# Performance work log

Hardware: AMD Instinct MI355X
Metric: run time of the kernel (lower is better)

The kernel has to match this reference:

```python
import jax, jax.numpy as jnp
import numpy as np

B, C, H, W = 16, 256, 32, 32
N_HEAD, DIM_HEAD = 8, 32  # dim_hidden = 256 == C


def setup_inputs() -> dict:
    key = jax.random.key(0)
    ks = jax.random.split(key, 9)
    s = 1.0 / np.sqrt(C)
    return {
        "x": jax.random.normal(ks[0], (B, C, H, W), dtype=jnp.float32),
        "w_q": jax.random.normal(ks[1], (C, C), dtype=jnp.float32) * s,
        "b_q": jnp.zeros((C,), dtype=jnp.float32),
        "w_k": jax.random.normal(ks[2], (C, C), dtype=jnp.float32) * s,
        "b_k": jnp.zeros((C,), dtype=jnp.float32),
        "w_v": jax.random.normal(ks[3], (C, C), dtype=jnp.float32) * s,
        "b_v": jnp.zeros((C,), dtype=jnp.float32),
        "w_o": jax.random.normal(ks[4], (C, C), dtype=jnp.float32) * s,
        "b_o": jnp.zeros((C,), dtype=jnp.float32),
    }


def reference(x, w_q, b_q, w_k, b_k, w_v, b_v, w_o, b_o):
    b, c, h, w = x.shape
    L = h * w
    scale = DIM_HEAD ** (-0.5)
    xf = x.reshape(b, c, L)  # [b, c, L]

    def proj(wm, bm):
        # 1x1 conv == per-position linear over channels
        y = jnp.einsum('oc,bcl->bol', wm, xf) + bm[None, :, None]
        return y.reshape(b, N_HEAD, DIM_HEAD, L)

    q = proj(w_q, b_q) * scale
    k = proj(w_k, b_k)
    v = proj(w_v, b_v)

    sim = jnp.einsum('bndl,bndm->bnlm', q, k)           # [b, n, L, L]
    att = jax.nn.softmax(sim, axis=-1)
    out = jnp.einsum('bnlm,bndm->bndl', att, v)         # [b, n, d, L]
    out = out.reshape(b, c, L)
    out = jnp.einsum('oc,bcl->bol', w_o, out) + b_o[None, :, None]
    return out.reshape(b, c, h, w)
```

## Files before the change

kernel.cpp:

```cpp
#include <hip/hip_runtime.h>
#include <hip/hip_bf16.h>
#include <math.h>

namespace {
constexpr int B_ = 16, C_ = 256, L_ = 1024, NH_ = 8, DH_ = 32;

typedef __attribute__((ext_vector_type(8))) short short8v;
typedef __attribute__((ext_vector_type(4))) float float4v;

__device__ __forceinline__ short f2bf(float f) {
    unsigned u = __builtin_bit_cast(unsigned, f);
    u += 0x7fffu + ((u >> 16) & 1u);
    return (short)(u >> 16);
}
__device__ __forceinline__ unsigned pkrn(float a, float b) {
    float2 f; f.x = a; f.y = b;
    __hip_bfloat162 h = __float22bfloat162_rn(f);
    unsigned u;
    __builtin_memcpy(&u, &h, sizeof(u));
    return u;
}
__device__ __forceinline__ void gld16(const short* g, short* l) {
    __builtin_amdgcn_global_load_lds(
        (const __attribute__((address_space(1))) unsigned*)g,
        (__attribute__((address_space(3))) unsigned*)l, 16, 0, 0);
}

__global__ __launch_bounds__(256, 4) void qkv_kernel(
    const float* __restrict__ X,
    const float* __restrict__ wq, const float* __restrict__ wk, const float* __restrict__ wv_,
    const float* __restrict__ bias0, const float* __restrict__ bias1, const float* __restrict__ bias2,
    float qscale, short* __restrict__ out0, short* __restrict__ out1, short* __restrict__ out2)
{
    const int lt = blockIdx.x, ot = blockIdx.y, b = blockIdx.z;
    const int t = threadIdx.x, wv = t >> 6, lane = t & 63;
    const int quad = lane >> 4, c = lane & 15;
    const int wo = (wv & 1) * 64;
    const int wl = (wv >> 1) * 32;

    __shared__ short sA[128 * 64];
    __shared__ short sB[64 * 64];

    float4v acc[4][2];
#pragma unroll
    for (int i = 0; i < 4; ++i)
#pragma unroll
        for (int j = 0; j < 2; ++j) acc[i][j] = (float4v)0.f;

    const int typ = ot >> 1;
    const float* Wsrc = (typ == 0) ? wq : (typ == 1) ? wk : wv_;
    const float* Wbase = Wsrc + (size_t)((ot & 1) * 128) * 256;

    const int srow = t >> 3, sseg = t & 7;
    const int seg = sseg ^ (srow & 7);

    for (int kk = 0; kk < 4; ++kk) {
        __syncthreads();
#pragma unroll
        for (int e = 0; e < 4; ++e) {
            const float* p = Wbase + (size_t)(e * 32 + srow) * 256 + kk * 64 + seg * 8;
            const float4 a0 = *(const float4*)p;
            const float4 a1 = *(const float4*)(p + 4);
            unsigned pk[4];
            pk[0] = pkrn(a0.x, a0.y); pk[1] = pkrn(a0.z, a0.w);
            pk[2] = pkrn(a1.x, a1.y); pk[3] = pkrn(a1.z, a1.w);
            *(uint4*)&sA[(e * 256 + t) * 8] = *(uint4*)pk;
        }
        {
            const int lrow = t & 63, w8 = t >> 6;
            const float* xcol = X + ((size_t)b * C_ + kk * 64 + w8 * 16) * L_ + lt * 64 + lrow;
            float vvv[16];
#pragma unroll
            for (int j = 0; j < 16; ++j) vvv[j] = xcol[(size_t)j * L_];
            unsigned pk[8];
#pragma unroll
            for (int j = 0; j < 8; ++j) pk[j] = pkrn(vvv[2 * j], vvv[2 * j + 1]);
            *(uint4*)&sB[(lrow * 8 + ((2 * w8)     ^ (lrow & 7))) * 8] = *(uint4*)&pk[0];
            *(uint4*)&sB[(lrow * 8 + ((2 * w8 + 1) ^ (lrow & 7))) * 8] = *(uint4*)&pk[4];
        }
        __syncthreads();

#pragma unroll
        for (int kc2 = 0; kc2 < 2; ++kc2) {
            short8v af[4], bf[2];
#pragma unroll
            for (int i = 0; i < 4; ++i) {
                const int row = wo + 16 * i + c;
                af[i] = *(const short8v*)&sA[row * 64 + (((kc2 * 4 + quad) ^ (c & 7)) * 8)];
            }
#pragma unroll
            for (int j = 0; j < 2; ++j) {
                const int row = wl + 16 * j + c;
                bf[j] = *(const short8v*)&sB[row * 64 + (((kc2 * 4 + quad) ^ (c & 7)) * 8)];
            }
#pragma unroll
            for (int i = 0; i < 4; ++i)
#pragma unroll
                for (int j = 0; j < 2; ++j)
                    acc[i][j] = __builtin_amdgcn_mfma_f32_16x16x32_bf16(af[i], bf[j], acc[i][j], 0, 0, 0);
        }
    }

    const int chbase = (ot & 1) * 128 + wo;
    const float* bp = (typ == 0) ? bias0 : (typ == 1) ? bias1 : bias2;
    const float sc = (typ == 0) ? qscale : 1.f;
    short* outp = (typ == 0) ? out0 : (typ == 1) ? out1 : out2;
    if (typ < 2) {
#pragma unroll
        for (int i = 0; i < 4; ++i) {
            const int ch0 = chbase + 16 * i + quad * 4;
            const int head = ch0 >> 5, d0 = ch0 & 31;
            float bias[4];
#pragma unroll
            for (int r = 0; r < 4; ++r) bias[r] = bp[ch0 + r];
#pragma unroll
            for (int j = 0; j < 2; ++j) {
                const int l = lt * 64 + wl + 16 * j + c;
                short4 sv;
                sv.x = f2bf((acc[i][j][0] + bias[0]) * sc);
                sv.y = f2bf((acc[i][j][1] + bias[1]) * sc);
                sv.z = f2bf((acc[i][j][2] + bias[2]) * sc);
                sv.w = f2bf((acc[i][j][3] + bias[3]) * sc);
                *(short4*)&outp[(((size_t)b * NH_ + head) * L_ + l) * 32 + d0] = sv;
            }
        }
    } else {
#pragma unroll
        for (int i = 0; i < 4; ++i)
#pragma unroll
            for (int r = 0; r < 4; ++r) {
                const int ch = chbase + 16 * i + quad * 4 + r;
                const float bias = bp[ch];
#pragma unroll
                for (int j = 0; j < 2; ++j)
                    outp[((size_t)b * C_ + ch) * L_ + lt * 64 + wl + 16 * j + c] =
                        f2bf(acc[i][j][r] + bias);
            }
    }
}

__global__ __launch_bounds__(256, 4) void ogemm_kernel(
    const float* __restrict__ Wo,
    const short* __restrict__ Bsrc,
    const float* __restrict__ bias,
    float* __restrict__ out)
{
    const int lt = blockIdx.x, ot = blockIdx.y, b = blockIdx.z;
    const int t = threadIdx.x, wv = t >> 6, lane = t & 63;
    const int quad = lane >> 4, c = lane & 15;
    const int wo = (wv & 1) * 64;
    const int wl = (wv >> 1) * 32;

    __shared__ short sA[128 * 64];
    __shared__ short sB[64 * 64];

    float4v acc[4][2];
#pragma unroll
    for (int i = 0; i < 4; ++i)
#pragma unroll
        for (int j = 0; j < 2; ++j) acc[i][j] = (float4v)0.f;

    const float* Wbase = Wo + (size_t)(ot * 128) * 256;
    const int srow = t >> 3, sseg = t & 7;
    const int seg = sseg ^ (srow & 7);

    for (int kk = 0; kk < 4; ++kk) {
        __syncthreads();
#pragma unroll
        for (int e = 0; e < 4; ++e) {
            const float* p = Wbase + (size_t)(e * 32 + srow) * 256 + kk * 64 + seg * 8;
            const float4 a0 = *(const float4*)p;
            const float4 a1 = *(const float4*)(p + 4);
            unsigned pk[4];
            pk[0] = pkrn(a0.x, a0.y); pk[1] = pkrn(a0.z, a0.w);
            pk[2] = pkrn(a1.x, a1.y); pk[3] = pkrn(a1.z, a1.w);
            *(uint4*)&sA[(e * 256 + t) * 8] = *(uint4*)pk;
        }
#pragma unroll
        for (int e = 0; e < 2; ++e)
            gld16(Bsrc + ((size_t)b * L_ + lt * 64 + e * 32 + srow) * 256 + kk * 64 + seg * 8,
                  &sB[(e * 256 + t) * 8]);
        __syncthreads();

#pragma unroll
        for (int kc2 = 0; kc2 < 2; ++kc2) {
            short8v af[4], bf[2];
#pragma unroll
            for (int i = 0; i < 4; ++i) {
                const int row = wo + 16 * i + c;
                af[i] = *(const short8v*)&sA[row * 64 + (((kc2 * 4 + quad) ^ (c & 7)) * 8)];
            }
#pragma unroll
            for (int j = 0; j < 2; ++j) {
                const int row = wl + 16 * j + c;
                bf[j] = *(const short8v*)&sB[row * 64 + (((kc2 * 4 + quad) ^ (c & 7)) * 8)];
            }
#pragma unroll
            for (int i = 0; i < 4; ++i)
#pragma unroll
                for (int j = 0; j < 2; ++j)
                    acc[i][j] = __builtin_amdgcn_mfma_f32_16x16x32_bf16(af[i], bf[j], acc[i][j], 0, 0, 0);
        }
    }

#pragma unroll
    for (int i = 0; i < 4; ++i)
#pragma unroll
        for (int r = 0; r < 4; ++r) {
            const int ch = ot * 128 + wo + 16 * i + quad * 4 + r;
            const float bs = bias[ch];
#pragma unroll
            for (int j = 0; j < 2; ++j)
                out[((size_t)b * C_ + ch) * L_ + lt * 64 + wl + 16 * j + c] =
                    acc[i][j][r] + bs;
        }
}

__global__ __launch_bounds__(256, 4) void attn_kernel(
    const short* __restrict__ qt,
    const short* __restrict__ kt,
    const short* __restrict__ vb,
    short* __restrict__ athi)
{
    const int flat = blockIdx.x;
    const int g = ((flat >> 6) << 3) | (flat & 7);
    const int chunk = (flat >> 3) & 7;
    const int b = g >> 3, h = g & 7;
    const int t = threadIdx.x;
    const int wv = t >> 6, lane = t & 63;
    const int quad = lane >> 4, c = lane & 15;
    const int lq0 = chunk * 128 + wv * 32;

    __shared__ __align__(16) short sK[2][64 * 32];
    __shared__ __align__(16) short sV[2][2][32 * 32];
    __shared__ __align__(16) short sPT[4][2][16][64];

    const size_t bh = (size_t)b * NH_ + h;
    const short* qbase = qt + (bh * L_) * 32;
    const short* kbase = kt + (bh * L_) * 32;
    const size_t vrow = (size_t)b * C_ + h * DH_;

    short8v qfrag[2];
#pragma unroll
    for (int qf = 0; qf < 2; ++qf)
        qfrag[qf] = *(const short8v*)(qbase + (size_t)(lq0 + qf * 16 + c) * 32 + quad * 8);

    float lp4[2][4];
#pragma unroll
    for (int qf = 0; qf < 2; ++qf)
#pragma unroll
        for (int r = 0; r < 4; ++r) lp4[qf][r] = 0.f;
    float4v o_acc[2][2];
#pragma unroll
    for (int qf = 0; qf < 2; ++qf) { o_acc[qf][0] = (float4v)0.f; o_acc[qf][1] = (float4v)0.f; }

    const int sseg = (t & 3) ^ ((t >> 3) & 3);
    const int rsw = (c >> 1) & 3;

    auto stage = [&](int m0, int buf) {
        gld16(kbase + (size_t)(m0 + (t >> 2)) * 32 + sseg * 8, &sK[buf][t * 8]);
        gld16(vb + (vrow + ((t >> 2) & 31)) * L_ + m0 + (t >> 7) * 32 + sseg * 8,
              (short*)sV[buf] + t * 8);
    };

    stage(0, 0);

    short8v vfp[2][2];

    for (int i = 0; i <= 16; ++i) {
        short8v kf[4], vf[2][2];
        if (i < 16) {
            __syncthreads();
            if (i < 15) stage((i + 1) * 64, (i + 1) & 1);
            const short* Kb = sK[i & 1];
            const short* Vb = (const short*)sV[i & 1];
#pragma unroll
            for (int kb = 0; kb < 4; ++kb)
                kf[kb] = *(const short8v*)&Kb[(kb * 16 + c) * 32 + ((quad ^ rsw) * 8)];
#pragma unroll
            for (int kc = 0; kc < 2; ++kc)
#pragma unroll
                for (int nb2 = 0; nb2 < 2; ++nb2)
                    vf[kc][nb2] = *(const short8v*)&Vb[kc * 1024 + (nb2 * 16 + c) * 32 + ((quad ^ rsw) * 8)];
        }

        if (i > 0) {
#pragma unroll
            for (int qf = 0; qf < 2; ++qf)
#pragma unroll
                for (int kc = 0; kc < 2; ++kc) {
                    const int G = (kc * 4 + quad) ^ (c & 7);
                    const short8v pf = *(const short8v*)&sPT[wv][qf][c][G * 8];
#pragma unroll
                    for (int nb2 = 0; nb2 < 2; ++nb2)
                        o_acc[qf][nb2] = __builtin_amdgcn_mfma_f32_16x16x32_bf16(vfp[kc][nb2], pf, o_acc[qf][nb2], 0, 0, 0);
                }
        }

        if (i < 16) {
            float4v st[2][4];
#pragma unroll
            for (int qf = 0; qf < 2; ++qf)
#pragma unroll
                for (int kb = 0; kb < 4; ++kb)
                    st[qf][kb] = __builtin_amdgcn_mfma_f32_16x16x32_bf16(kf[kb], qfrag[qf], (float4v)0.f, 0, 0, 0);
#pragma unroll
            for (int qf = 0; qf < 2; ++qf)
#pragma unroll
                for (int kb = 0; kb < 4; ++kb) {
                    float p[4];
#pragma unroll
                    for (int r = 0; r < 4; ++r) {
                        p[r] = __builtin_amdgcn_exp2f(st[qf][kb][r]);
                        lp4[qf][r] += p[r];
                    }
                    uint2 w;
                    w.x = pkrn(p[0], p[1]);
                    w.y = pkrn(p[2], p[3]);
                    const int Gw = (kb * 2 + (quad >> 1)) ^ (c & 7);
                    *(uint2*)&sPT[wv][qf][c][Gw * 8 + (quad & 1) * 4] = w;
                }
#pragma unroll
            for (int kc = 0; kc < 2; ++kc)
#pragma unroll
                for (int nb2 = 0; nb2 < 2; ++nb2) vfp[kc][nb2] = vf[kc][nb2];
        }
    }

#pragma unroll
    for (int qf = 0; qf < 2; ++qf) {
        float l = (lp4[qf][0] + lp4[qf][1]) + (lp4[qf][2] + lp4[qf][3]);
        l += __shfl_xor(l, 16);
        l += __shfl_xor(l, 32);
        const float inv = 1.f / l;
#pragma unroll
        for (int nb2 = 0; nb2 < 2; ++nb2) {
            short4 sv;
            sv.x = f2bf(o_acc[qf][nb2][0] * inv);
            sv.y = f2bf(o_acc[qf][nb2][1] * inv);
            sv.z = f2bf(o_acc[qf][nb2][2] * inv);
            sv.w = f2bf(o_acc[qf][nb2][3] * inv);
            *(short4*)&athi[((size_t)b * L_ + lq0 + qf * 16 + c) * C_ + h * DH_ + nb2 * 16 + quad * 4] = sv;
        }
    }
}

}

extern "C" void kernel_launch(void* const* d_in, const int* in_sizes, int n_in,
                              void* d_out, int out_size, void* d_ws, size_t ws_size,
                              hipStream_t stream) {
    const float* x   = (const float*)d_in[0];
    const float* w_q = (const float*)d_in[1];
    const float* b_q = (const float*)d_in[2];
    const float* w_k = (const float*)d_in[3];
    const float* b_k = (const float*)d_in[4];
    const float* w_v = (const float*)d_in[5];
    const float* b_v = (const float*)d_in[6];
    const float* w_o = (const float*)d_in[7];
    const float* b_o = (const float*)d_in[8];
    float* out = (float*)d_out;

    const size_t NT = (size_t)B_ * L_ * C_;
    short* qt   = (short*)d_ws;
    short* kt   = qt + NT;
    short* vb   = kt + NT;
    short* athi = vb + NT;

    const float scale_q = 0.17677669529663687f * 1.4426950408889634f;

    qkv_kernel<<<dim3(L_ / 64, 6, B_), 256, 0, stream>>>(
        x, w_q, w_k, w_v, b_q, b_k, b_v, scale_q, qt, kt, vb);
    attn_kernel<<<dim3(1024), 256, 0, stream>>>(qt, kt, vb, athi);
    ogemm_kernel<<<dim3(L_ / 64, 2, B_), 256, 0, stream>>>(
        w_o, athi, b_o, out);
}
```

Baseline: 140.1 us.

## Pre-convert weights to bf16 once and widen QKV tile to 256 channels

Adds a small kernel that converts all four weight matrices to bf16 once per call, so the GEMM kernels load them with direct global-to-LDS copies instead of converting fp32 per block. The QKV kernel now computes all 256 output channels of one projection per block (8x2 accumulator tiles per wave), which halves how often each X tile is reloaded and converted. In exchange it adds a kernel launch, uses more LDS and registers (occupancy hint lowered to 3), and launches half as many QKV blocks.

```diff
diff --git a/kernel.cpp b/kernel.cpp
--- a/kernel.cpp
+++ b/kernel.cpp
@@ -26,46 +26,52 @@
         (__attribute__((address_space(3))) unsigned*)l, 16, 0, 0);
 }
 
-__global__ __launch_bounds__(256, 4) void qkv_kernel(
-    const float* __restrict__ X,
-    const float* __restrict__ wq, const float* __restrict__ wk, const float* __restrict__ wv_,
+__global__ __launch_bounds__(256) void prepw_kernel(
+    const float* __restrict__ wq, const float* __restrict__ wk,
+    const float* __restrict__ wv, const float* __restrict__ wo,
+    short* __restrict__ WA, short* __restrict__ WoA)
+{
+    const int g4 = blockIdx.x * 256 + threadIdx.x;
+    const int o = g4 >> 6, cc = (g4 & 63) * 4;
+    const float* src = (o < 256) ? wq : (o < 512) ? wk : (o < 768) ? wv : wo;
+    const float4 v = *(const float4*)&src[(size_t)(o & 255) * 256 + cc];
+    short4 s;
+    s.x = f2bf(v.x); s.y = f2bf(v.y); s.z = f2bf(v.z); s.w = f2bf(v.w);
+    short* dst = (o < 768) ? &WA[(size_t)o * 256 + cc]
+                           : &WoA[(size_t)(o - 768) * 256 + cc];
+    *(short4*)dst = s;
+}
+
+__global__ __launch_bounds__(256, 3) void qkv_kernel(
+    const float* __restrict__ X, const short* __restrict__ WA,
     const float* __restrict__ bias0, const float* __restrict__ bias1, const float* __restrict__ bias2,
     float qscale, short* __restrict__ out0, short* __restrict__ out1, short* __restrict__ out2)
 {
-    const int lt = blockIdx.x, ot = blockIdx.y, b = blockIdx.z;
+    const int lt = blockIdx.x, typ = blockIdx.y, b = blockIdx.z;
     const int t = threadIdx.x, wv = t >> 6, lane = t & 63;
     const int quad = lane >> 4, c = lane & 15;
-    const int wo = (wv & 1) * 64;
+    const int wo = (wv & 1) * 128;
     const int wl = (wv >> 1) * 32;
 
-    __shared__ short sA[128 * 64];
+    __shared__ short sA[256 * 64];
     __shared__ short sB[64 * 64];
 
-    float4v acc[4][2];
-#pragma unroll
-    for (int i = 0; i < 4; ++i)
+    float4v acc[8][2];
+#pragma unroll
+    for (int i = 0; i < 8; ++i)
 #pragma unroll
         for (int j = 0; j < 2; ++j) acc[i][j] = (float4v)0.f;
 
-    const int typ = ot >> 1;
-    const float* Wsrc = (typ == 0) ? wq : (typ == 1) ? wk : wv_;
-    const float* Wbase = Wsrc + (size_t)((ot & 1) * 128) * 256;
-
+    const short* Arow = WA + (size_t)(typ * 256) * 256;
     const int srow = t >> 3, sseg = t & 7;
     const int seg = sseg ^ (srow & 7);
 
     for (int kk = 0; kk < 4; ++kk) {
         __syncthreads();
 #pragma unroll
-        for (int e = 0; e < 4; ++e) {
-            const float* p = Wbase + (size_t)(e * 32 + srow) * 256 + kk * 64 + seg * 8;
-            const float4 a0 = *(const float4*)p;
-            const float4 a1 = *(const float4*)(p + 4);
-            unsigned pk[4];
-            pk[0] = pkrn(a0.x, a0.y); pk[1] = pkrn(a0.z, a0.w);
-            pk[2] = pkrn(a1.x, a1.y); pk[3] = pkrn(a1.z, a1.w);
-            *(uint4*)&sA[(e * 256 + t) * 8] = *(uint4*)pk;
-        }
+        for (int e = 0; e < 8; ++e)
+            gld16(Arow + (size_t)(e * 32 + srow) * 256 + kk * 64 + seg * 8,
+                  &sA[(e * 256 + t) * 8]);
         {
             const int lrow = t & 63, w8 = t >> 6;
             const float* xcol = X + ((size_t)b * C_ + kk * 64 + w8 * 16) * L_ + lt * 64 + lrow;
@@ -82,33 +88,37 @@
 
 #pragma unroll
         for (int kc2 = 0; kc2 < 2; ++kc2) {
-            short8v af[4], bf[2];
-#pragma unroll
-            for (int i = 0; i < 4; ++i) {
-                const int row = wo + 16 * i + c;
-                af[i] = *(const short8v*)&sA[row * 64 + (((kc2 * 4 + quad) ^ (c & 7)) * 8)];
-            }
+            short8v bf[2];
 #pragma unroll
             for (int j = 0; j < 2; ++j) {
                 const int row = wl + 16 * j + c;
                 bf[j] = *(const short8v*)&sB[row * 64 + (((kc2 * 4 + quad) ^ (c & 7)) * 8)];
             }
 #pragma unroll
-            for (int i = 0; i < 4; ++i)
-#pragma unroll
-                for (int j = 0; j < 2; ++j)
-                    acc[i][j] = __builtin_amdgcn_mfma_f32_16x16x32_bf16(af[i], bf[j], acc[i][j], 0, 0, 0);
-        }
-    }
-
-    const int chbase = (ot & 1) * 128 + wo;
+            for (int half = 0; half < 2; ++half) {
+                short8v af[4];
+#pragma unroll
+                for (int i2 = 0; i2 < 4; ++i2) {
+                    const int row = wo + (half * 4 + i2) * 16 + c;
+                    af[i2] = *(const short8v*)&sA[row * 64 + (((kc2 * 4 + quad) ^ (c & 7)) * 8)];
+                }
+#pragma unroll
+                for (int i2 = 0; i2 < 4; ++i2)
+#pragma unroll
+                    for (int j = 0; j < 2; ++j)
+                        acc[half * 4 + i2][j] = __builtin_amdgcn_mfma_f32_16x16x32_bf16(
+                            af[i2], bf[j], acc[half * 4 + i2][j], 0, 0, 0);
+            }
+        }
+    }
+
     const float* bp = (typ == 0) ? bias0 : (typ == 1) ? bias1 : bias2;
     const float sc = (typ == 0) ? qscale : 1.f;
     short* outp = (typ == 0) ? out0 : (typ == 1) ? out1 : out2;
     if (typ < 2) {
 #pragma unroll
-        for (int i = 0; i < 4; ++i) {
-            const int ch0 = chbase + 16 * i + quad * 4;
+        for (int i = 0; i < 8; ++i) {
+            const int ch0 = wo + 16 * i + quad * 4;
             const int head = ch0 >> 5, d0 = ch0 & 31;
             float bias[4];
 #pragma unroll
@@ -126,10 +136,10 @@
         }
     } else {
 #pragma unroll
-        for (int i = 0; i < 4; ++i)
+        for (int i = 0; i < 8; ++i)
 #pragma unroll
             for (int r = 0; r < 4; ++r) {
-                const int ch = chbase + 16 * i + quad * 4 + r;
+                const int ch = wo + 16 * i + quad * 4 + r;
                 const float bias = bp[ch];
 #pragma unroll
                 for (int j = 0; j < 2; ++j)
@@ -140,7 +150,7 @@
 }
 
 __global__ __launch_bounds__(256, 4) void ogemm_kernel(
-    const float* __restrict__ Wo,
+    const short* __restrict__ WoA,
     const short* __restrict__ Bsrc,
     const float* __restrict__ bias,
     float* __restrict__ out)
@@ -160,22 +170,16 @@
 #pragma unroll
         for (int j = 0; j < 2; ++j) acc[i][j] = (float4v)0.f;
 
-    const float* Wbase = Wo + (size_t)(ot * 128) * 256;
+    const short* Arow = WoA + (size_t)(ot * 128) * 256;
     const int srow = t >> 3, sseg = t & 7;
     const int seg = sseg ^ (srow & 7);
 
     for (int kk = 0; kk < 4; ++kk) {
         __syncthreads();
 #pragma unroll
-        for (int e = 0; e < 4; ++e) {
-            const float* p = Wbase + (size_t)(e * 32 + srow) * 256 + kk * 64 + seg * 8;
-            const float4 a0 = *(const float4*)p;
-            const float4 a1 = *(const float4*)(p + 4);
-            unsigned pk[4];
-            pk[0] = pkrn(a0.x, a0.y); pk[1] = pkrn(a0.z, a0.w);
-            pk[2] = pkrn(a1.x, a1.y); pk[3] = pkrn(a1.z, a1.w);
-            *(uint4*)&sA[(e * 256 + t) * 8] = *(uint4*)pk;
-        }
+        for (int e = 0; e < 4; ++e)
+            gld16(Arow + (size_t)(e * 32 + srow) * 256 + kk * 64 + seg * 8,
+                  &sA[(e * 256 + t) * 8]);
 #pragma unroll
         for (int e = 0; e < 2; ++e)
             gld16(Bsrc + ((size_t)b * L_ + lt * 64 + e * 32 + srow) * 256 + kk * 64 + seg * 8,
@@ -362,16 +366,19 @@
     float* out = (float*)d_out;
 
     const size_t NT = (size_t)B_ * L_ * C_;
-    short* qt   = (short*)d_ws;
+    short* WA   = (short*)d_ws;
+    short* WoA  = WA + 768 * 256;
+    short* qt   = WoA + 256 * 256;
     short* kt   = qt + NT;
     short* vb   = kt + NT;
     short* athi = vb + NT;
 
     const float scale_q = 0.17677669529663687f * 1.4426950408889634f;
 
-    qkv_kernel<<<dim3(L_ / 64, 6, B_), 256, 0, stream>>>(
-        x, w_q, w_k, w_v, b_q, b_k, b_v, scale_q, qt, kt, vb);
+    prepw_kernel<<<dim3(256), 256, 0, stream>>>(w_q, w_k, w_v, w_o, WA, WoA);
+    qkv_kernel<<<dim3(L_ / 64, 3, B_), 256, 0, stream>>>(
+        x, WA, b_q, b_k, b_v, scale_q, qt, kt, vb);
     attn_kernel<<<dim3(1024), 256, 0, stream>>>(qt, kt, vb, athi);
     ogemm_kernel<<<dim3(L_ / 64, 2, B_), 256, 0, stream>>>(
-        w_o, athi, b_o, out);
-}
+        WoA, athi, b_o, out);
+}
```

Measured after the change: 134.4 us (median of 2 runs). 1.04x faster.
